# Kernel tuning notes

Measured on AMD Instinct MI355X. Metric: run time of the kernel, lower is better.

The kernel has to match this reference:

```python
import jax, jax.numpy as jnp
import numpy as np

D_MODEL = 1024
D_STATE = 16
D_CONV = 4
D_INNER = 2 * D_MODEL          # expand * d_model
DT_RANK = (D_MODEL + 15) // 16 # ceil(d_model/16) = 64
BATCH, SEQLEN = 2, 1024


def setup_inputs() -> dict:
    key = jax.random.key(0)
    ks = jax.random.split(key, 8)
    s = lambda k, shape, scale=0.02: (jax.random.normal(k, shape, jnp.float32) * scale)
    return {
        "hidden_states": jax.random.normal(ks[0], (BATCH, SEQLEN, D_MODEL), jnp.float32),
        "in_proj_w": s(ks[1], (2 * D_INNER, D_MODEL)),
        "conv_w": s(ks[2], (D_INNER, 1, D_CONV), 0.3),   # depthwise conv kernel (O, I/groups=1, K)
        "conv_b": jnp.zeros((D_INNER,), jnp.float32),
        "x_proj_w": s(ks[3], (DT_RANK + 2 * D_STATE, D_INNER)),
        "dt_proj_w": s(ks[4], (D_INNER, DT_RANK), 0.1),
        # inverse-softplus of small dt values, like the torch init
        "dt_proj_b": jax.random.uniform(ks[5], (D_INNER,), jnp.float32, minval=-5.0, maxval=-2.0),
        "A_log": jnp.log(jnp.broadcast_to(jnp.arange(1, D_STATE + 1, dtype=jnp.float32), (D_INNER, D_STATE))),
        "D": jnp.ones((D_INNER,), jnp.float32),
        "out_proj_w": s(ks[6], (D_MODEL, D_INNER)),
    }


def _forward(hidden_states, in_proj_w, conv_w, conv_b, x_proj_w,
             dt_proj_w, dt_proj_b, A_log, D, out_proj_w):
    B, L, _ = hidden_states.shape
    # in_proj -> split into x, z
    xz = hidden_states @ in_proj_w.T                      # [B, L, 2*d_inner]
    x, z = jnp.split(xz, 2, axis=-1)
    # causal depthwise conv1d (pad left d_conv-1, then take first L) + SiLU
    xc = jnp.transpose(x, (0, 2, 1))                      # [B, d_inner, L]
    xc = jax.lax.conv_general_dilated(
        xc, conv_w, window_strides=(1,), padding=[(D_CONV - 1, 0)],
        feature_group_count=D_INNER,
        dimension_numbers=("NCH", "OIH", "NCH")) + conv_b[None, :, None]
    xc = jax.nn.silu(xc)
    u = jnp.transpose(xc, (0, 2, 1)).astype(jnp.float32)  # [B, L, d_inner]
    # x_proj -> dt_low, B, C
    x_dbl = u @ x_proj_w.T                                # [B, L, dt_rank + 2*d_state]
    dt_low, Bp, Cp = jnp.split(x_dbl, [DT_RANK, DT_RANK + D_STATE], axis=-1)
    dt = dt_low @ dt_proj_w.T + dt_proj_b                 # [B, L, d_inner]
    # NOTE: original adds dt_proj.bias AGAIN as delta_bias inside the scan, then softplus
    delta = jax.nn.softplus(dt + dt_proj_b)
    A = -jnp.exp(A_log.astype(jnp.float32))               # [d_inner, d_state]
    # discretization
    dA = jnp.exp(jnp.einsum("bld,dn->lbdn", delta, A))    # [L, B, d, n]
    dBu = jnp.einsum("bld,bln,bld->lbdn", delta, Bp.astype(jnp.float32), u)
    C_t = jnp.transpose(Cp.astype(jnp.float32), (1, 0, 2))  # [L, B, n]

    def step(state, inp):
        a, b, c = inp
        state = a * state + b                             # [B, d, n]
        y = jnp.einsum("bdn,bn->bd", state, c)
        return state, y

    x0 = jnp.zeros((B, D_INNER, D_STATE), jnp.float32)
    _, ys = jax.lax.scan(step, x0, (dA, dBu, C_t))        # ys: [L, B, d]
    y = jnp.transpose(ys, (1, 0, 2))                      # [B, L, d]
    y = y + u * D.astype(jnp.float32)                     # skip connection
    y = y * jax.nn.silu(z.astype(jnp.float32))            # gating
    y = y.astype(hidden_states.dtype)
    return y @ out_proj_w.T                               # [B, L, d_model]


def reference(hidden_states, in_proj_w, conv_w, conv_b, x_proj_w,
              dt_proj_w, dt_proj_b, A_log, D, out_proj_w):
    return _forward(hidden_states, in_proj_w, conv_w, conv_b, x_proj_w,
                    dt_proj_w, dt_proj_b, A_log, D, out_proj_w)
```

## Files before the change

### kernel.cpp

```cpp
#include <hip/hip_runtime.h>
#include <hip/hip_bf16.h>
#include <math.h>

#define BATCH   2
#define SEQLEN  1024
#define DMODEL  1024
#define DINNER  2048
#define DSTATE  16
#define DTRANK  64
#define XPAD    128
#define MROWS   (BATCH*SEQLEN)
#define NSEG2   64
#define SEGL2   (SEQLEN/NSEG2)
#define XP_SPLIT  8
#define OUT_SPLIT 2

typedef float    f32x4  __attribute__((ext_vector_type(4)));
typedef _Float16 f16x8  __attribute__((ext_vector_type(8)));
typedef _Float16 f16x4  __attribute__((ext_vector_type(4)));

template<int EPI>
__global__ __launch_bounds__(256) void pgemm64(
    const _Float16* __restrict__ A, int lda,
    const _Float16* __restrict__ W, int ldw,
    float* __restrict__ C, int ldc, int K,
    const float* __restrict__ bias, _Float16* __restrict__ C16, size_t zstride)
{
  constexpr int APS = 520;
  constexpr int BPS = 1032;
  __shared__ _Float16 As[2][8 * APS];
  __shared__ _Float16 Bs[2][8 * BPS];

  const int t  = threadIdx.x;
  const int m0 = blockIdx.y * 64, n0 = blockIdx.x * 128;
  const int kchunk = K / gridDim.z;
  const int kbeg = blockIdx.z * kchunk;
  const int nIter = kchunk / 64;

  const int kb = t & 7;
  const int r0 = t >> 3;
  const _Float16* gA = A + (size_t)(m0 + r0) * lda + kbeg + kb * 8;
  const _Float16* gB = W + (size_t)(n0 + r0) * ldw + kbeg + kb * 8;
  const size_t a32 = (size_t)32 * lda;
  const size_t b32 = (size_t)32 * ldw;
  const int aoff = kb * APS + r0 * 8;
  const int boff = kb * BPS + r0 * 8;

  {
    f16x8 a0 = *(const f16x8*)(gA);
    f16x8 a1 = *(const f16x8*)(gA + a32);
    f16x8 b0 = *(const f16x8*)(gB);
    f16x8 b1 = *(const f16x8*)(gB + b32);
    f16x8 b2 = *(const f16x8*)(gB + 2 * b32);
    f16x8 b3 = *(const f16x8*)(gB + 3 * b32);
    gA += 64; gB += 64;
    *(f16x8*)&As[0][aoff]       = a0;
    *(f16x8*)&As[0][aoff + 256] = a1;
    *(f16x8*)&Bs[0][boff]       = b0;
    *(f16x8*)&Bs[0][boff + 256] = b1;
    *(f16x8*)&Bs[0][boff + 512] = b2;
    *(f16x8*)&Bs[0][boff + 768] = b3;
  }

  const int lane = t & 63, wvi = t >> 6;
  const int wn = wvi * 32;
  const int lm = lane & 15, lk = lane >> 4;

  f32x4 acc[4][2] = {};

  for (int it = 0; it < nIter; ++it) {
    __syncthreads();
    const bool more = (it + 1 < nIter);
    f16x8 a0, a1, b0, b1, b2, b3;
    if (more) {
      a0 = *(const f16x8*)(gA);
      a1 = *(const f16x8*)(gA + a32);
      b0 = *(const f16x8*)(gB);
      b1 = *(const f16x8*)(gB + b32);
      b2 = *(const f16x8*)(gB + 2 * b32);
      b3 = *(const f16x8*)(gB + 3 * b32);
      gA += 64; gB += 64;
    }
    const int cb = it & 1;
#pragma unroll
    for (int s = 0; s < 2; ++s) {
      f16x8 av[4], bv[2];
#pragma unroll
      for (int i = 0; i < 4; ++i)
        av[i] = *(const f16x8*)&As[cb][(s * 4 + lk) * APS + (i * 16 + lm) * 8];
#pragma unroll
      for (int j = 0; j < 2; ++j)
        bv[j] = *(const f16x8*)&Bs[cb][(s * 4 + lk) * BPS + (wn + j * 16 + lm) * 8];
#pragma unroll
      for (int i = 0; i < 4; ++i)
#pragma unroll
        for (int j = 0; j < 2; ++j)
          acc[i][j] = __builtin_amdgcn_mfma_f32_16x16x32_f16(av[i], bv[j], acc[i][j], 0, 0, 0);
    }
    if (more) {
      const int nb = (it + 1) & 1;
      *(f16x8*)&As[nb][aoff]       = a0;
      *(f16x8*)&As[nb][aoff + 256] = a1;
      *(f16x8*)&Bs[nb][boff]       = b0;
      *(f16x8*)&Bs[nb][boff + 256] = b1;
      *(f16x8*)&Bs[nb][boff + 512] = b2;
      *(f16x8*)&Bs[nb][boff + 768] = b3;
    }
  }

  float* Cz = C + (size_t)blockIdx.z * zstride;
#pragma unroll
  for (int i = 0; i < 4; ++i) {
    const int mrow = m0 + i * 16 + lk * 4;
#pragma unroll
    for (int j = 0; j < 2; ++j) {
      const int col = n0 + wn + j * 16 + lm;
#pragma unroll
      for (int r = 0; r < 4; ++r) {
        float v = acc[i][j][r];
        size_t off = (size_t)(mrow + r) * ldc + col;
        if constexpr (EPI == 0) {
          Cz[off] = v;
        } else {
          float x = v + 2.f * bias[col];
          float sp = (x > 20.f) ? x : __logf(1.f + __expf(x));
          C16[off] = (_Float16)sp;
        }
      }
    }
  }
}

template<int EPI>
__global__ __launch_bounds__(256) void pgemm128(
    const _Float16* __restrict__ A, int lda,
    const _Float16* __restrict__ W, int ldw,
    float* __restrict__ C, int ldc, int K,
    _Float16* __restrict__ C16, size_t zstride)
{
  constexpr int PS = 1032;
  __shared__ _Float16 As[2][8 * PS];
  __shared__ _Float16 Bs[2][8 * PS];

  const int t  = threadIdx.x;
  const int m0 = blockIdx.y * 128, n0 = blockIdx.x * 128;
  const int kchunk = K / gridDim.z;
  const int kbeg = blockIdx.z * kchunk;
  const int nIter = kchunk / 64;

  const int kb = t & 7;
  const int r0 = t >> 3;
  const _Float16* gA = A + (size_t)(m0 + r0) * lda + kbeg + kb * 8;
  const _Float16* gB = W + (size_t)(n0 + r0) * ldw + kbeg + kb * 8;
  const size_t a32 = (size_t)32 * lda;
  const size_t b32 = (size_t)32 * ldw;
  const int soff = kb * PS + r0 * 8;

  {
    f16x8 ar[4], br[4];
#pragma unroll
    for (int j = 0; j < 4; ++j) {
      ar[j] = *(const f16x8*)(gA + j * a32);
      br[j] = *(const f16x8*)(gB + j * b32);
    }
    gA += 64; gB += 64;
#pragma unroll
    for (int j = 0; j < 4; ++j) {
      *(f16x8*)&As[0][soff + j * 256] = ar[j];
      *(f16x8*)&Bs[0][soff + j * 256] = br[j];
    }
  }

  const int lane = t & 63, wvi = t >> 6;
  const int wm = (wvi >> 1) * 64, wn = (wvi & 1) * 64;
  const int lm = lane & 15, lk = lane >> 4;

  f32x4 acc[4][4] = {};

  for (int it = 0; it < nIter; ++it) {
    __syncthreads();
    const bool more = (it + 1 < nIter);
    f16x8 ar[4], br[4];
    if (more) {
#pragma unroll
      for (int j = 0; j < 4; ++j) {
        ar[j] = *(const f16x8*)(gA + j * a32);
        br[j] = *(const f16x8*)(gB + j * b32);
      }
      gA += 64; gB += 64;
    }
    const int cb = it & 1;
#pragma unroll
    for (int s = 0; s < 2; ++s) {
      f16x8 av[4], bv[4];
#pragma unroll
      for (int i = 0; i < 4; ++i)
        av[i] = *(const f16x8*)&As[cb][(s * 4 + lk) * PS + (wm + i * 16 + lm) * 8];
#pragma unroll
      for (int j = 0; j < 4; ++j)
        bv[j] = *(const f16x8*)&Bs[cb][(s * 4 + lk) * PS + (wn + j * 16 + lm) * 8];
#pragma unroll
      for (int i = 0; i < 4; ++i)
#pragma unroll
        for (int j = 0; j < 4; ++j)
          acc[i][j] = __builtin_amdgcn_mfma_f32_16x16x32_f16(av[i], bv[j], acc[i][j], 0, 0, 0);
    }
    if (more) {
      const int nb = (it + 1) & 1;
#pragma unroll
      for (int j = 0; j < 4; ++j) {
        *(f16x8*)&As[nb][soff + j * 256] = ar[j];
        *(f16x8*)&Bs[nb][soff + j * 256] = br[j];
      }
    }
  }

  float* Cz = C + (size_t)blockIdx.z * zstride;
#pragma unroll
  for (int i = 0; i < 4; ++i) {
    const int mrow = m0 + wm + i * 16 + lk * 4;
#pragma unroll
    for (int j = 0; j < 4; ++j) {
      const int col = n0 + wn + j * 16 + lm;
#pragma unroll
      for (int r = 0; r < 4; ++r) {
        float v = acc[i][j][r];
        size_t off = (size_t)(mrow + r) * ldc + col;
        if constexpr (EPI == 0) {
          Cz[off] = v;
        } else {
          C16[off] = (_Float16)v;
        }
      }
    }
  }
}

#define R0 (MROWS * DMODEL / 4)
#define R1 (2 * DINNER * DMODEL / 4)
#define R2 (DMODEL * DINNER / 4)
#define R3 (DINNER * DTRANK / 4)
#define R4 (XPAD * DINNER / 4)
#define F2H_TOTAL (R0 + R1 + R2 + R3 + R4)

__global__ __launch_bounds__(256) void f2h_all(
    const float* __restrict__ hid, const float* __restrict__ w_in,
    const float* __restrict__ w_out, const float* __restrict__ w_dt,
    const float* __restrict__ w_xp,
    _Float16* __restrict__ hid16, _Float16* __restrict__ w_in16,
    _Float16* __restrict__ w_out16, _Float16* __restrict__ w_dt16,
    _Float16* __restrict__ w_xp16)
{
  int i = blockIdx.x * 256 + threadIdx.x;
  const float* src; _Float16* dst; int off;
  if (i < R0)                     { src = hid;   dst = hid16;   off = i; }
  else if (i < R0+R1)             { src = w_in;  dst = w_in16;  off = i - R0; }
  else if (i < R0+R1+R2)          { src = w_out; dst = w_out16; off = i - (R0+R1); }
  else if (i < R0+R1+R2+R3)       { src = w_dt;  dst = w_dt16;  off = i - (R0+R1+R2); }
  else if (i < F2H_TOTAL) {
    off = i - (R0+R1+R2+R3);
    int r = (off * 4) >> 11;
    f16x4 h = {0, 0, 0, 0};
    if (r < 96) {
      float4 v = ((const float4*)w_xp)[off];
      h = (f16x4){(_Float16)v.x, (_Float16)v.y, (_Float16)v.z, (_Float16)v.w};
    }
    ((f16x4*)w_xp16)[off] = h;
    return;
  } else return;
  float4 v = ((const float4*)src)[off];
  ((f16x4*)dst)[off] = (f16x4){(_Float16)v.x, (_Float16)v.y, (_Float16)v.z, (_Float16)v.w};
}

__global__ __launch_bounds__(256) void reduce_xdbl(
    const float* __restrict__ part,
    float* __restrict__ xdbl32, _Float16* __restrict__ xdbl16)
{
  int i = blockIdx.x * 256 + threadIdx.x;
  f32x4 s = ((const f32x4*)part)[i];
#pragma unroll
  for (int z = 1; z < XP_SPLIT; ++z)
    s += ((const f32x4*)part)[(size_t)z * (MROWS * XPAD / 4) + i];
  ((f32x4*)xdbl32)[i] = s;
  int col4 = (i & 31) * 4;
  if (col4 < DTRANK) {
    int row = i >> 5;
    *(f16x4*)&xdbl16[(size_t)row * DTRANK + col4] =
        (f16x4){(_Float16)s.x, (_Float16)s.y, (_Float16)s.z, (_Float16)s.w};
  }
}

__global__ __launch_bounds__(256) void reduce_out(
    const float* __restrict__ part, float* __restrict__ out)
{
  int i = blockIdx.x * 256 + threadIdx.x;
  f32x4 s = ((const f32x4*)part)[i];
#pragma unroll
  for (int z = 1; z < OUT_SPLIT; ++z)
    s += ((const f32x4*)part)[(size_t)z * (MROWS * DMODEL / 4) + i];
  ((f32x4*)out)[i] = s;
}

__global__ __launch_bounds__(256) void conv_silu(
    const _Float16* __restrict__ xz16,
    const float* __restrict__ conv_w,
    const float* __restrict__ conv_b,
    _Float16* __restrict__ u16)
{
  const int idx = blockIdx.x * 256 + threadIdx.x;
  const int d   = idx & (DINNER - 1);
  const int row = idx >> 11;
  const int l   = row & (SEQLEN - 1);
  float s = conv_b[d];
#pragma unroll
  for (int k = 0; k < 4; ++k) {
    int lt = l + k - 3;
    if (lt >= 0)
      s = fmaf((float)xz16[(size_t)(row + k - 3) * (2 * DINNER) + d],
               conv_w[d * 4 + k], s);
  }
  float v = s / (1.f + __expf(-s));
  u16[idx] = (_Float16)v;
}

__global__ __launch_bounds__(256) void scan_pe(
    const _Float16* __restrict__ delta16,
    const _Float16* __restrict__ u16,
    const float* __restrict__ x_dbl,
    const float* __restrict__ A_log,
    float* __restrict__ pbuf, float* __restrict__ ebuf)
{
  const int t = threadIdx.x;
  const int d = blockIdx.x * 256 + t;
  const int b   = blockIdx.y >> 6;
  const int seg = blockIdx.y & 63;
  const int row0 = b * SEQLEN + seg * SEGL2;

  float A_dn[DSTATE];
#pragma unroll
  for (int q = 0; q < 4; ++q) {
    f32x4 a4 = *(const f32x4*)&A_log[(size_t)d * DSTATE + q * 4];
#pragma unroll
    for (int e = 0; e < 4; ++e) A_dn[q * 4 + e] = -__expf(a4[e]);
  }

  __shared__ __align__(16) float Bl[SEGL2 * DSTATE];
  if (t < 64) {
    int i = t >> 2, n4 = (t & 3) * 4;
    *(f32x4*)&Bl[i * DSTATE + n4] =
        *(const f32x4*)&x_dbl[(size_t)(row0 + i) * XPAD + DTRANK + n4];
  }
  __syncthreads();

  float E[DSTATE];
#pragma unroll
  for (int n = 0; n < DSTATE; ++n) E[n] = 0.f;
  float S = 0.f;

  for (int i = 0; i < SEGL2; ++i) {
    const size_t ro = (size_t)(row0 + i) * DINNER + d;
    float dv = (float)delta16[ro];
    float uv = (float)u16[ro];
    float du = dv * uv;
    S += dv;
#pragma unroll
    for (int n = 0; n < DSTATE; ++n) {
      float dA = __expf(dv * A_dn[n]);
      E[n] = fmaf(dA, E[n], du * Bl[i * DSTATE + n]);
    }
  }

  const size_t base = ((size_t)(b * NSEG2 + seg) * DSTATE) * DINNER + d;
#pragma unroll
  for (int n = 0; n < DSTATE; ++n) {
    pbuf[base + (size_t)n * DINNER] = __expf(S * A_dn[n]);
    ebuf[base + (size_t)n * DINNER] = E[n];
  }
}

__global__ __launch_bounds__(256) void scan_mid(
    const float* __restrict__ pbuf, const float* __restrict__ ebuf,
    float* __restrict__ cbuf)
{
  const int idx = blockIdx.x * 256 + threadIdx.x;
  const int d = idx & (DINNER - 1);
  const int n = (idx >> 11) & 15;
  const int b = idx >> 15;
  float s = 0.f;
  for (int seg = 0; seg < NSEG2; ++seg) {
    const size_t off = ((size_t)(b * NSEG2 + seg) * DSTATE + n) * DINNER + d;
    cbuf[off] = s;
    s = fmaf(pbuf[off], s, ebuf[off]);
  }
}

__global__ __launch_bounds__(256) void scan_y(
    const _Float16* __restrict__ delta16,
    const _Float16* __restrict__ u16,
    const _Float16* __restrict__ xz16,
    const float* __restrict__ x_dbl,
    const float* __restrict__ A_log,
    const float* __restrict__ Dp,
    const float* __restrict__ cbuf,
    _Float16* __restrict__ y16)
{
  const int t = threadIdx.x;
  const int d = blockIdx.x * 256 + t;
  const int b   = blockIdx.y >> 6;
  const int seg = blockIdx.y & 63;
  const int row0 = b * SEQLEN + seg * SEGL2;

  float A_dn[DSTATE];
#pragma unroll
  for (int q = 0; q < 4; ++q) {
    f32x4 a4 = *(const f32x4*)&A_log[(size_t)d * DSTATE + q * 4];
#pragma unroll
    for (int e = 0; e < 4; ++e) A_dn[q * 4 + e] = -__expf(a4[e]);
  }
  const float Dv = Dp[d];

  __shared__ __align__(16) float Bl[SEGL2 * DSTATE];
  __shared__ __align__(16) float Cl[SEGL2 * DSTATE];
  if (t < 64) {
    int i = t >> 2, n4 = (t & 3) * 4;
    *(f32x4*)&Bl[i * DSTATE + n4] =
        *(const f32x4*)&x_dbl[(size_t)(row0 + i) * XPAD + DTRANK + n4];
  } else if (t < 128) {
    int u = t - 64;
    int i = u >> 2, n4 = (u & 3) * 4;
    *(f32x4*)&Cl[i * DSTATE + n4] =
        *(const f32x4*)&x_dbl[(size_t)(row0 + i) * XPAD + DTRANK + DSTATE + n4];
  }
  __syncthreads();

  float s[DSTATE];
  {
    const size_t base = ((size_t)(b * NSEG2 + seg) * DSTATE) * DINNER + d;
#pragma unroll
    for (int n = 0; n < DSTATE; ++n) s[n] = cbuf[base + (size_t)n * DINNER];
  }

  for (int i = 0; i < SEGL2; ++i) {
    const size_t ro = (size_t)(row0 + i) * DINNER + d;
    float dv = (float)delta16[ro];
    float uv = (float)u16[ro];
    float zv = (float)xz16[(size_t)(row0 + i) * (2 * DINNER) + DINNER + d];
    float du = dv * uv;
    float y = 0.f;
#pragma unroll
    for (int n = 0; n < DSTATE; ++n) {
      float dA = __expf(dv * A_dn[n]);
      s[n] = fmaf(dA, s[n], du * Bl[i * DSTATE + n]);
      y = fmaf(s[n], Cl[i * DSTATE + n], y);
    }
    y = fmaf(uv, Dv, y);
    y *= zv / (1.f + __expf(-zv));
    y16[ro] = (_Float16)y;
  }
}

extern "C" void kernel_launch(void* const* d_in, const int* in_sizes, int n_in,
                              void* d_out, int out_size, void* d_ws, size_t ws_size,
                              hipStream_t stream)
{
  const float* hidden     = (const float*)d_in[0];
  const float* in_proj_w  = (const float*)d_in[1];
  const float* conv_w     = (const float*)d_in[2];
  const float* conv_b     = (const float*)d_in[3];
  const float* x_proj_w   = (const float*)d_in[4];
  const float* dt_proj_w  = (const float*)d_in[5];
  const float* dt_proj_b  = (const float*)d_in[6];
  const float* A_log      = (const float*)d_in[7];
  const float* Dp         = (const float*)d_in[8];
  const float* out_proj_w = (const float*)d_in[9];
  float* out = (float*)d_out;

  char* p = (char*)d_ws;
  _Float16* xz16    = (_Float16*)p;  p += (size_t)MROWS * 2 * DINNER * 2;
  _Float16* u16     = (_Float16*)p;  p += (size_t)MROWS * DINNER * 2;
  float*    xdbl32  = (float*)p;     p += (size_t)MROWS * XPAD * 4;
  _Float16* delta16 = (_Float16*)p;  p += (size_t)MROWS * DINNER * 2;
  _Float16* h16     = (_Float16*)p;  p += (size_t)MROWS * DMODEL * 2;
  _Float16* win16   = (_Float16*)p;  p += (size_t)2 * DINNER * DMODEL * 2;
  _Float16* wout16  = (_Float16*)p;  p += (size_t)DMODEL * DINNER * 2;
  _Float16* wdt16   = (_Float16*)p;  p += (size_t)DINNER * DTRANK * 2;
  _Float16* wxp16   = (_Float16*)p;  p += (size_t)XPAD * DINNER * 2;
  _Float16* xdbl16  = (_Float16*)p;  p += (size_t)MROWS * DTRANK * 2;
  _Float16* y16     = (_Float16*)p;  p += (size_t)MROWS * DINNER * 2;
  float*    pbuf    = (float*)p;     p += (size_t)BATCH * NSEG2 * DSTATE * DINNER * 4;
  float*    ebuf    = (float*)p;     p += (size_t)BATCH * NSEG2 * DSTATE * DINNER * 4;
  float*    cbuf    = (float*)p;     p += (size_t)BATCH * NSEG2 * DSTATE * DINNER * 4;
  float*    xp_part  = (float*)delta16;
  float*    out_part = (float*)xz16;

  f2h_all<<<(F2H_TOTAL + 255) / 256, 256, 0, stream>>>(
      hidden, in_proj_w, out_proj_w, dt_proj_w, x_proj_w,
      h16, win16, wout16, wdt16, wxp16);

  pgemm128<4><<<dim3(4096 / 128, MROWS / 128, 1), 256, 0, stream>>>(
      h16, DMODEL, win16, DMODEL, nullptr, 4096, DMODEL, xz16, 0);

  conv_silu<<<(MROWS * DINNER) / 256, 256, 0, stream>>>(xz16, conv_w, conv_b, u16);

  pgemm64<0><<<dim3(1, MROWS / 64, XP_SPLIT), 256, 0, stream>>>(
      u16, DINNER, wxp16, DINNER, xp_part, XPAD, DINNER, nullptr, nullptr,
      (size_t)MROWS * XPAD);

  reduce_xdbl<<<(MROWS * XPAD / 4) / 256, 256, 0, stream>>>(xp_part, xdbl32, xdbl16);

  pgemm64<2><<<dim3(DINNER / 128, MROWS / 64, 1), 256, 0, stream>>>(
      xdbl16, DTRANK, wdt16, DTRANK, nullptr, DINNER, DTRANK, dt_proj_b, delta16, 0);

  scan_pe<<<dim3(DINNER / 256, BATCH * NSEG2), 256, 0, stream>>>(
      delta16, u16, xdbl32, A_log, pbuf, ebuf);
  scan_mid<<<(BATCH * DSTATE * DINNER) / 256, 256, 0, stream>>>(pbuf, ebuf, cbuf);
  scan_y<<<dim3(DINNER / 256, BATCH * NSEG2), 256, 0, stream>>>(
      delta16, u16, xz16, xdbl32, A_log, Dp, cbuf, y16);

  pgemm128<0><<<dim3(DMODEL / 128, MROWS / 128, OUT_SPLIT), 256, 0, stream>>>(
      y16, DINNER, wout16, DINNER, out_part, DMODEL, DINNER, nullptr,
      (size_t)MROWS * DMODEL);

  reduce_out<<<(MROWS * DMODEL / 4) / 256, 256, 0, stream>>>(out_part, out);
}
```

Before: 229.3 us.

## Fuse dt_proj GEMM and softplus into scan_pe, halve scan segment count

Removes the separate dt_proj GEMM launch and the fp16 conversion of dt_proj weights and x_dbl. scan_pe now computes delta per row with an fp32 dot product over the 64 dt_rank values held in shared memory, applies softplus with the doubled bias, and writes delta16 for scan_y. The segment count drops from 64 to 32 so each block covers longer segments, which cuts pbuf/ebuf/cbuf traffic and scan_mid work but gives the scan kernels half as many blocks. Each thread now keeps 64 dt weights in registers, which may reduce occupancy.

```diff
diff --git a/kernel.cpp b/kernel.cpp
--- a/kernel.cpp
+++ b/kernel.cpp
@@ -10,7 +10,7 @@
 #define DTRANK  64
 #define XPAD    128
 #define MROWS   (BATCH*SEQLEN)
-#define NSEG2   64
+#define NSEG2   32
 #define SEGL2   (SEQLEN/NSEG2)
 #define XP_SPLIT  8
 #define OUT_SPLIT 2
@@ -116,17 +116,8 @@
     for (int j = 0; j < 2; ++j) {
       const int col = n0 + wn + j * 16 + lm;
 #pragma unroll
-      for (int r = 0; r < 4; ++r) {
-        float v = acc[i][j][r];
-        size_t off = (size_t)(mrow + r) * ldc + col;
-        if constexpr (EPI == 0) {
-          Cz[off] = v;
-        } else {
-          float x = v + 2.f * bias[col];
-          float sp = (x > 20.f) ? x : __logf(1.f + __expf(x));
-          C16[off] = (_Float16)sp;
-        }
-      }
+      for (int r = 0; r < 4; ++r)
+        Cz[(size_t)(mrow + r) * ldc + col] = acc[i][j][r];
     }
   }
 }
@@ -239,26 +230,22 @@
 #define R0 (MROWS * DMODEL / 4)
 #define R1 (2 * DINNER * DMODEL / 4)
 #define R2 (DMODEL * DINNER / 4)
-#define R3 (DINNER * DTRANK / 4)
 #define R4 (XPAD * DINNER / 4)
-#define F2H_TOTAL (R0 + R1 + R2 + R3 + R4)
+#define F2H_TOTAL (R0 + R1 + R2 + R4)
 
 __global__ __launch_bounds__(256) void f2h_all(
     const float* __restrict__ hid, const float* __restrict__ w_in,
-    const float* __restrict__ w_out, const float* __restrict__ w_dt,
-    const float* __restrict__ w_xp,
+    const float* __restrict__ w_out, const float* __restrict__ w_xp,
     _Float16* __restrict__ hid16, _Float16* __restrict__ w_in16,
-    _Float16* __restrict__ w_out16, _Float16* __restrict__ w_dt16,
-    _Float16* __restrict__ w_xp16)
+    _Float16* __restrict__ w_out16, _Float16* __restrict__ w_xp16)
 {
   int i = blockIdx.x * 256 + threadIdx.x;
   const float* src; _Float16* dst; int off;
   if (i < R0)                     { src = hid;   dst = hid16;   off = i; }
   else if (i < R0+R1)             { src = w_in;  dst = w_in16;  off = i - R0; }
   else if (i < R0+R1+R2)          { src = w_out; dst = w_out16; off = i - (R0+R1); }
-  else if (i < R0+R1+R2+R3)       { src = w_dt;  dst = w_dt16;  off = i - (R0+R1+R2); }
   else if (i < F2H_TOTAL) {
-    off = i - (R0+R1+R2+R3);
+    off = i - (R0+R1+R2);
     int r = (off * 4) >> 11;
     f16x4 h = {0, 0, 0, 0};
     if (r < 96) {
@@ -274,7 +261,7 @@
 
 __global__ __launch_bounds__(256) void reduce_xdbl(
     const float* __restrict__ part,
-    float* __restrict__ xdbl32, _Float16* __restrict__ xdbl16)
+    float* __restrict__ xdbl32)
 {
   int i = blockIdx.x * 256 + threadIdx.x;
   f32x4 s = ((const f32x4*)part)[i];
@@ -282,12 +269,6 @@
   for (int z = 1; z < XP_SPLIT; ++z)
     s += ((const f32x4*)part)[(size_t)z * (MROWS * XPAD / 4) + i];
   ((f32x4*)xdbl32)[i] = s;
-  int col4 = (i & 31) * 4;
-  if (col4 < DTRANK) {
-    int row = i >> 5;
-    *(f16x4*)&xdbl16[(size_t)row * DTRANK + col4] =
-        (f16x4){(_Float16)s.x, (_Float16)s.y, (_Float16)s.z, (_Float16)s.w};
-  }
 }
 
 __global__ __launch_bounds__(256) void reduce_out(
@@ -324,17 +305,25 @@
 }
 
 __global__ __launch_bounds__(256) void scan_pe(
-    const _Float16* __restrict__ delta16,
     const _Float16* __restrict__ u16,
     const float* __restrict__ x_dbl,
     const float* __restrict__ A_log,
-    float* __restrict__ pbuf, float* __restrict__ ebuf)
+    const float* __restrict__ dt_w,
+    const float* __restrict__ dt_b,
+    float* __restrict__ pbuf, float* __restrict__ ebuf,
+    _Float16* __restrict__ delta16)
 {
   const int t = threadIdx.x;
   const int d = blockIdx.x * 256 + t;
-  const int b   = blockIdx.y >> 6;
-  const int seg = blockIdx.y & 63;
+  const int b   = blockIdx.y >> 5;
+  const int seg = blockIdx.y & 31;
   const int row0 = b * SEQLEN + seg * SEGL2;
+
+  f32x4 w[16];
+#pragma unroll
+  for (int q = 0; q < 16; ++q)
+    w[q] = *(const f32x4*)&dt_w[(size_t)d * DTRANK + q * 4];
+  const float b2 = 2.f * dt_b[d];
 
   float A_dn[DSTATE];
 #pragma unroll
@@ -344,11 +333,21 @@
     for (int e = 0; e < 4; ++e) A_dn[q * 4 + e] = -__expf(a4[e]);
   }
 
+  __shared__ __align__(16) float xd[SEGL2 * 64];
   __shared__ __align__(16) float Bl[SEGL2 * DSTATE];
-  if (t < 64) {
-    int i = t >> 2, n4 = (t & 3) * 4;
-    *(f32x4*)&Bl[i * DSTATE + n4] =
-        *(const f32x4*)&x_dbl[(size_t)(row0 + i) * XPAD + DTRANK + n4];
+  {
+#pragma unroll
+    for (int k = 0; k < 2; ++k) {
+      int idx = t * 2 + k;
+      int i = idx >> 4, c4 = (idx & 15) * 4;
+      *(f32x4*)&xd[i * 64 + c4] =
+          *(const f32x4*)&x_dbl[(size_t)(row0 + i) * XPAD + c4];
+    }
+    if (t < 128) {
+      int i = t >> 2, n4 = (t & 3) * 4;
+      *(f32x4*)&Bl[i * DSTATE + n4] =
+          *(const f32x4*)&x_dbl[(size_t)(row0 + i) * XPAD + DTRANK + n4];
+    }
   }
   __syncthreads();
 
@@ -358,8 +357,19 @@
   float S = 0.f;
 
   for (int i = 0; i < SEGL2; ++i) {
+    float a = b2;
+#pragma unroll
+    for (int q = 0; q < 16; ++q) {
+      f32x4 x4 = *(const f32x4*)&xd[i * 64 + q * 4];
+      a = fmaf(x4[0], w[q][0], a);
+      a = fmaf(x4[1], w[q][1], a);
+      a = fmaf(x4[2], w[q][2], a);
+      a = fmaf(x4[3], w[q][3], a);
+    }
+    float dv = (a > 20.f) ? a : __logf(1.f + __expf(a));
     const size_t ro = (size_t)(row0 + i) * DINNER + d;
-    float dv = (float)delta16[ro];
+    delta16[ro] = (_Float16)dv;
+    dv = (float)(_Float16)dv;
     float uv = (float)u16[ro];
     float du = dv * uv;
     S += dv;
@@ -406,8 +416,8 @@
 {
   const int t = threadIdx.x;
   const int d = blockIdx.x * 256 + t;
-  const int b   = blockIdx.y >> 6;
-  const int seg = blockIdx.y & 63;
+  const int b   = blockIdx.y >> 5;
+  const int seg = blockIdx.y & 31;
   const int row0 = b * SEQLEN + seg * SEGL2;
 
   float A_dn[DSTATE];
@@ -421,12 +431,12 @@
 
   __shared__ __align__(16) float Bl[SEGL2 * DSTATE];
   __shared__ __align__(16) float Cl[SEGL2 * DSTATE];
-  if (t < 64) {
+  if (t < 128) {
     int i = t >> 2, n4 = (t & 3) * 4;
     *(f32x4*)&Bl[i * DSTATE + n4] =
         *(const f32x4*)&x_dbl[(size_t)(row0 + i) * XPAD + DTRANK + n4];
-  } else if (t < 128) {
-    int u = t - 64;
+  } else {
+    int u = t - 128;
     int i = u >> 2, n4 = (u & 3) * 4;
     *(f32x4*)&Cl[i * DSTATE + n4] =
         *(const f32x4*)&x_dbl[(size_t)(row0 + i) * XPAD + DTRANK + DSTATE + n4];
@@ -483,9 +493,7 @@
   _Float16* h16     = (_Float16*)p;  p += (size_t)MROWS * DMODEL * 2;
   _Float16* win16   = (_Float16*)p;  p += (size_t)2 * DINNER * DMODEL * 2;
   _Float16* wout16  = (_Float16*)p;  p += (size_t)DMODEL * DINNER * 2;
-  _Float16* wdt16   = (_Float16*)p;  p += (size_t)DINNER * DTRANK * 2;
   _Float16* wxp16   = (_Float16*)p;  p += (size_t)XPAD * DINNER * 2;
-  _Float16* xdbl16  = (_Float16*)p;  p += (size_t)MROWS * DTRANK * 2;
   _Float16* y16     = (_Float16*)p;  p += (size_t)MROWS * DINNER * 2;
   float*    pbuf    = (float*)p;     p += (size_t)BATCH * NSEG2 * DSTATE * DINNER * 4;
   float*    ebuf    = (float*)p;     p += (size_t)BATCH * NSEG2 * DSTATE * DINNER * 4;
@@ -494,8 +502,8 @@
   float*    out_part = (float*)xz16;
 
   f2h_all<<<(F2H_TOTAL + 255) / 256, 256, 0, stream>>>(
-      hidden, in_proj_w, out_proj_w, dt_proj_w, x_proj_w,
-      h16, win16, wout16, wdt16, wxp16);
+      hidden, in_proj_w, out_proj_w, x_proj_w,
+      h16, win16, wout16, wxp16);
 
   pgemm128<4><<<dim3(4096 / 128, MROWS / 128, 1), 256, 0, stream>>>(
       h16, DMODEL, win16, DMODEL, nullptr, 4096, DMODEL, xz16, 0);
@@ -506,13 +514,10 @@
       u16, DINNER, wxp16, DINNER, xp_part, XPAD, DINNER, nullptr, nullptr,
       (size_t)MROWS * XPAD);
 
-  reduce_xdbl<<<(MROWS * XPAD / 4) / 256, 256, 0, stream>>>(xp_part, xdbl32, xdbl16);
-
-  pgemm64<2><<<dim3(DINNER / 128, MROWS / 64, 1), 256, 0, stream>>>(
-      xdbl16, DTRANK, wdt16, DTRANK, nullptr, DINNER, DTRANK, dt_proj_b, delta16, 0);
+  reduce_xdbl<<<(MROWS * XPAD / 4) / 256, 256, 0, stream>>>(xp_part, xdbl32);
 
   scan_pe<<<dim3(DINNER / 256, BATCH * NSEG2), 256, 0, stream>>>(
-      delta16, u16, xdbl32, A_log, pbuf, ebuf);
+      u16, xdbl32, A_log, dt_proj_w, dt_proj_b, pbuf, ebuf, delta16);
   scan_mid<<<(BATCH * DSTATE * DINNER) / 256, 256, 0, stream>>>(pbuf, ebuf, cbuf);
   scan_y<<<dim3(DINNER / 256, BATCH * NSEG2), 256, 0, stream>>>(
       delta16, u16, xz16, xdbl32, A_log, Dp, cbuf, y16);
```

Result: no change. 230.8 us (+0.7%).
